# Optimization experiments

Hardware: AMD Instinct MI355X
Metric: run time of the kernel (lower is better)

## Reference

```python
import jax, jax.numpy as jnp
import numpy as np
from jax import lax

H = W = 496
K = 5            # gabor kernel size
WIN = 16         # window_size
STRIDE = 16
PATCH = 32
GAMMA = 0.5
PSI = np.pi / 2
THETAS = np.array([np.pi/8, np.pi/4, 3*np.pi/8, np.pi/2, 5*np.pi/8, 6*np.pi/8, 7*np.pi/8, np.pi], dtype=np.float32)


def setup_inputs() -> dict:
    key = jax.random.key(0)
    k1, k2, k3 = jax.random.split(key, 3)
    img = jax.random.normal(k1, (1, 1, H, W), dtype=jnp.float32)
    sigmas = jax.random.uniform(k2, (1, 3), dtype=jnp.float32) * 10.0   # nn.Parameter(rand*10)
    lambdas = jax.random.uniform(k3, (1, 3), dtype=jnp.float32) * np.pi  # nn.Parameter(rand*pi)
    return {"img": img, "sigmas": sigmas, "lambdas": lambdas}


def _gabor_bank(sigmas, lambdas):
    # axes: (sigma, lambda, theta, ky, kx)
    idx = jnp.arange(K, dtype=jnp.float32) - (K - 1) / 2.0
    sig = sigmas[0][:, None, None, None, None]          # [3,1,1,1,1]
    lam = lambdas[0][None, :, None, None, None]         # [1,3,1,1,1]
    th = jnp.asarray(THETAS)[None, None, :, None, None] # [1,1,8,1,1]
    y = idx[None, None, None, :, None]
    x = idx[None, None, None, None, :]
    sigma_x = sig
    sigma_y = sig / GAMMA
    sin_t, cos_t = jnp.sin(th), jnp.cos(th)
    y_theta = -x * sin_t + y * cos_t
    x_theta = x * cos_t + y * sin_t
    gb = jnp.exp(-0.5 * (x_theta**2 / sigma_x**2 + y_theta**2 / sigma_y**2)) \
         * jnp.cos(2.0 * np.pi * x_theta / lam + PSI)
    return gb.reshape(-1, 1, K, K)  # [72,1,5,5]


def reference(img, sigmas, lambdas):
    gb = _gabor_bank(sigmas, lambdas)
    res = lax.conv_general_dilated(
        img, gb, window_strides=(1, 1), padding=[(K // 2, K // 2)] * 2,
        dimension_numbers=("NCHW", "OIHW", "NCHW"))          # [1,72,H,W]
    res = res.reshape(1, 9, 8, H, W).max(axis=2)              # max over 8 thetas -> [1,9,H,W]
    out = res[0]                                              # [9,H,W]

    # find_maxima: per-channel threshold at 5*mean, zero below (torch.nn.Threshold)
    mean = out.mean(axis=(1, 2), keepdims=True)
    thr = jnp.where(out > mean * 5.0, out, 0.0)

    nw = H // STRIDE                                          # 31
    windows = thr.reshape(9, nw, WIN, nw, WIN).transpose(0, 1, 3, 2, 4).reshape(9, nw * nw, WIN * WIN)
    is_max = jnp.argmax(windows, axis=2) == (WIN * WIN) // 2  # [9, 961]

    w_idx = jnp.arange(nw * nw)
    rows = w_idx // nw * STRIDE + WIN // 2
    cols = w_idx % nw * STRIDE + WIN // 2

    # describe: zero-pad by 16, gather 32x32 patch at each candidate keypoint for every channel
    pad = jnp.pad(out, ((0, 0), (16, 16), (16, 16)))
    pr = rows[:, None, None] + jnp.arange(PATCH)[None, :, None]   # [961,32,1]
    pc = cols[:, None, None] + jnp.arange(PATCH)[None, None, :]   # [961,1,32]
    patches = pad[:, pr, pc]                                      # [9,961,32,32]

    # keep patches only for detected keypoints with nonzero content (original skips zero patches)
    valid_kp = jnp.any(is_max, axis=0)                            # [961]
    nonzero = jnp.any(patches != 0, axis=(2, 3))                  # [9,961]
    mask = (valid_kp[None, :] & nonzero).astype(patches.dtype)
    patches = patches * mask[:, :, None, None]
    return patches
```

## Files before the change

kernel.cpp:

```cpp
#include <hip/hip_runtime.h>
#include <math.h>

#define HH 496
#define WW 496
#define HWSZ (HH*WW)
#define NW 31
#define NWIN (NW*NW)

__constant__ float c_thetas[8] = {
    0.39269908169872414f, 0.7853981633974483f, 1.1780972450961724f,
    1.5707963267948966f,  1.9634954084936207f, 2.356194490192345f,
    2.748893571891069f,   3.141592653589793f};

__global__ void bank_kernel(const float* __restrict__ sigmas,
                            const float* __restrict__ lambdas,
                            float* __restrict__ filt,
                            float* __restrict__ meanacc) {
    int idx = threadIdx.x + blockIdx.x * blockDim.x;
    if (idx >= 1800) {
        if (idx < 1809) meanacc[(idx - 1800) * 16] = 0.0f;
        return;
    }
    int f = idx / 25, k = idx % 25;
    int dy = k / 5, dx = k % 5;
    int s = f / 24, rem = f % 24, l = rem / 8, t = rem % 8;
    float sig = sigmas[s], lam = lambdas[l], th = c_thetas[t];
    float y = (float)dy - 2.0f, x = (float)dx - 2.0f;
    float st = sinf(th), ct = cosf(th);
    float yt = -x * st + y * ct;
    float xt =  x * ct + y * st;
    float sx2 = sig * sig;
    float sy2 = 4.0f * sig * sig;
    float g = expf(-0.5f * (xt * xt / sx2 + yt * yt / sy2)) *
              cosf(6.28318530717958647692f * xt / lam + 1.5707963267948966f);
    filt[k * 72 + f] = g;
}

#define FMAS(FP, P) \
    a0  = fmaf(P, (FP)[0],  a0);  a1  = fmaf(P, (FP)[1],  a1);  \
    a2  = fmaf(P, (FP)[2],  a2);  a3  = fmaf(P, (FP)[3],  a3);  \
    a4  = fmaf(P, (FP)[4],  a4);  a5  = fmaf(P, (FP)[5],  a5);  \
    a6  = fmaf(P, (FP)[6],  a6);  a7  = fmaf(P, (FP)[7],  a7);  \
    a8  = fmaf(P, (FP)[8],  a8);  a9  = fmaf(P, (FP)[9],  a9);  \
    a10 = fmaf(P, (FP)[10], a10); a11 = fmaf(P, (FP)[11], a11); \
    a12 = fmaf(P, (FP)[12], a12); a13 = fmaf(P, (FP)[13], a13); \
    a14 = fmaf(P, (FP)[14], a14); a15 = fmaf(P, (FP)[15], a15); \
    a16 = fmaf(P, (FP)[16], a16); a17 = fmaf(P, (FP)[17], a17); \
    a18 = fmaf(P, (FP)[18], a18); a19 = fmaf(P, (FP)[19], a19); \
    a20 = fmaf(P, (FP)[20], a20); a21 = fmaf(P, (FP)[21], a21); \
    a22 = fmaf(P, (FP)[22], a22); a23 = fmaf(P, (FP)[23], a23);

#define STEP(K, DY, DX) { \
    float pix = tile[tbase + (DY)*20 + (DX)]; \
    const float* fp = fbase + (K)*72; \
    FMAS(fp, pix) }

__global__ __launch_bounds__(256) void conv_kernel(
    const float* __restrict__ img, const float* __restrict__ filt,
    float* __restrict__ out, float* __restrict__ meanacc) {
    __shared__ float tile[20 * 20];
    __shared__ float red[4][3];
    int tid = threadIdx.x;
    int tx = tid & 15, ty = tid >> 4;
    int bx = blockIdx.x, by = blockIdx.y, cg = blockIdx.z;

    for (int i = tid; i < 400; i += 256) {
        int tY = i / 20, tX = i % 20;
        int gy = by * 16 + tY - 2, gx = bx * 16 + tX - 2;
        float v = 0.0f;
        if (gy >= 0 && gy < HH && gx >= 0 && gx < WW) v = img[gy * WW + gx];
        tile[i] = v;
    }
    __syncthreads();

    float a0=0,a1=0,a2=0,a3=0,a4=0,a5=0,a6=0,a7=0,a8=0,a9=0,a10=0,a11=0,
          a12=0,a13=0,a14=0,a15=0,a16=0,a17=0,a18=0,a19=0,a20=0,a21=0,a22=0,a23=0;
    int tbase = ty * 20 + tx;
    const float* fbase = filt + cg * 24;

    STEP( 0,0,0) STEP( 1,0,1) STEP( 2,0,2) STEP( 3,0,3) STEP( 4,0,4)
    STEP( 5,1,0) STEP( 6,1,1) STEP( 7,1,2) STEP( 8,1,3) STEP( 9,1,4)
    STEP(10,2,0) STEP(11,2,1) STEP(12,2,2) STEP(13,2,3) STEP(14,2,4)
    STEP(15,3,0) STEP(16,3,1) STEP(17,3,2) STEP(18,3,3) STEP(19,3,4)
    STEP(20,4,0) STEP(21,4,1) STEP(22,4,2) STEP(23,4,3) STEP(24,4,4)

    int y = by * 16 + ty, x = bx * 16 + tx;

    float m0 = fmaxf(fmaxf(fmaxf(a0,a1),fmaxf(a2,a3)),fmaxf(fmaxf(a4,a5),fmaxf(a6,a7)));
    float m1 = fmaxf(fmaxf(fmaxf(a8,a9),fmaxf(a10,a11)),fmaxf(fmaxf(a12,a13),fmaxf(a14,a15)));
    float m2 = fmaxf(fmaxf(fmaxf(a16,a17),fmaxf(a18,a19)),fmaxf(fmaxf(a20,a21),fmaxf(a22,a23)));

    out[(cg * 3 + 0) * HWSZ + y * WW + x] = m0;
    out[(cg * 3 + 1) * HWSZ + y * WW + x] = m1;
    out[(cg * 3 + 2) * HWSZ + y * WW + x] = m2;

#define RED(CC, MV) { \
        float s = MV; \
        s += __shfl_down(s, 32, 64); s += __shfl_down(s, 16, 64); \
        s += __shfl_down(s,  8, 64); s += __shfl_down(s,  4, 64); \
        s += __shfl_down(s,  2, 64); s += __shfl_down(s,  1, 64); \
        if ((tid & 63) == 0) red[tid >> 6][CC] = s; }
    RED(0, m0) RED(1, m1) RED(2, m2)
    __syncthreads();
    if (tid < 3)
        atomicAdd(&meanacc[(cg * 3 + tid) * 16],
                  red[0][tid] + red[1][tid] + red[2][tid] + red[3][tid]);
}

__global__ __launch_bounds__(256) void patch_kernel(
    const float* __restrict__ out, const float* __restrict__ meanacc,
    float* __restrict__ dst) {
    int w = blockIdx.x;
    int r = w / NW, cl = w % NW;
    int tid = threadIdx.x;
    __shared__ int lds_and[4];
    __shared__ int lds_or[4];

    int wy = tid >> 4, wx = tid & 15;
    int rowbase = (r * 16 + wy) * WW + cl * 16 + wx;
    int cbase   = (r * 16 + 8) * WW + cl * 16;
    int okmask = 0;
#pragma unroll
    for (int c = 0; c < 9; c++) {
        float m5 = meanacc[c * 16] * (5.0f / (float)HWSZ);
        float v  = out[c * HWSZ + rowbase];
        float vc = out[c * HWSZ + cbase];
        float thr  = (v  > m5) ? v  : 0.0f;
        float thrc = (vc > m5) ? vc : 0.0f;
        bool ok = (tid < 128) ? (thr < thrc) : (thr <= thrc);
        okmask |= (ok ? 1 : 0) << c;
    }
#pragma unroll
    for (int off = 1; off < 64; off <<= 1) okmask &= __shfl_xor(okmask, off, 64);
    if ((tid & 63) == 0) lds_and[tid >> 6] = okmask;

    int i = tid >> 3;
    int jg = (tid & 7) << 2;
    int row = r * 16 + i - 8;
    int col = cl * 16 + jg - 8;
    bool inb = (row >= 0 && row < HH && col >= 0 && col + 3 < WW);
    size_t pbase = (size_t)row * WW + col;
    int nzmask = 0;
    float4 p0, p1, p2, p3, p4, p5, p6, p7, p8;
#define LOADP(C, V) { \
        V = make_float4(0.f, 0.f, 0.f, 0.f); \
        if (inb) V = *(const float4*)(out + (size_t)(C) * HWSZ + pbase); \
        if (V.x != 0.f || V.y != 0.f || V.z != 0.f || V.w != 0.f) nzmask |= 1 << (C); }
    LOADP(0,p0) LOADP(1,p1) LOADP(2,p2) LOADP(3,p3) LOADP(4,p4)
    LOADP(5,p5) LOADP(6,p6) LOADP(7,p7) LOADP(8,p8)

#pragma unroll
    for (int off = 1; off < 64; off <<= 1) nzmask |= __shfl_xor(nzmask, off, 64);
    if ((tid & 63) == 0) lds_or[tid >> 6] = nzmask;
    __syncthreads();

    int am = lds_and[0] & lds_and[1] & lds_and[2] & lds_and[3];
    int om = lds_or[0] | lds_or[1] | lds_or[2] | lds_or[3];
    bool valid = (am != 0);

    size_t dbase = (size_t)w * 1024 + i * 32 + jg;
#define STOREP(C, V) { \
        float mk = (valid && ((om >> (C)) & 1)) ? 1.0f : 0.0f; \
        V.x *= mk; V.y *= mk; V.z *= mk; V.w *= mk; \
        *(float4*)(dst + (size_t)(C) * NWIN * 1024 + dbase) = V; }
    STOREP(0,p0) STOREP(1,p1) STOREP(2,p2) STOREP(3,p3) STOREP(4,p4)
    STOREP(5,p5) STOREP(6,p6) STOREP(7,p7) STOREP(8,p8)
}

extern "C" void kernel_launch(void* const* d_in, const int* in_sizes, int n_in,
                              void* d_out, int out_size, void* d_ws, size_t ws_size,
                              hipStream_t stream) {
    const float* img     = (const float*)d_in[0];
    const float* sigmas  = (const float*)d_in[1];
    const float* lambdas = (const float*)d_in[2];
    float* ws = (float*)d_ws;
    float* filt    = ws;
    float* meanacc = ws + 2048;
    float* outb    = ws + 4096;

    bank_kernel<<<8, 256, 0, stream>>>(sigmas, lambdas, filt, meanacc);
    conv_kernel<<<dim3(NW, NW, 3), 256, 0, stream>>>(img, filt, outb, meanacc);
    patch_kernel<<<NWIN, 256, 0, stream>>>(outb, meanacc, (float*)d_out);
}
```

Baseline: 122.1 us.

## Fuse convolution and patch extraction into one cooperative kernel with grid sync

The separate conv and patch kernels are merged into one cooperative kernel launched with a fixed grid of 496 blocks of 512 threads. Each block covers two 16x16 windows and computes all 9 channel groups per thread. The per-channel mean is accumulated with atomics, and a grid-wide sync then lets the same blocks run the thresholding, argmax check and patch gather. This removes one kernel launch and the gap between kernels. In exchange, far fewer threads run the convolution, each doing three times the work, and it adds the cost of a grid barrier and of a cooperative launch.

```diff
diff --git a/kernel.cpp b/kernel.cpp
--- a/kernel.cpp
+++ b/kernel.cpp
@@ -1,5 +1,8 @@
 #include <hip/hip_runtime.h>
+#include <hip/hip_cooperative_groups.h>
 #include <math.h>
+
+namespace cg = cooperative_groups;
 
 #define HH 496
 #define WW 496
@@ -51,78 +54,93 @@
     a22 = fmaf(P, (FP)[22], a22); a23 = fmaf(P, (FP)[23], a23);
 
 #define STEP(K, DY, DX) { \
-    float pix = tile[tbase + (DY)*20 + (DX)]; \
+    float pix = mytile[tbase + (DY)*20 + (DX)]; \
     const float* fp = fbase + (K)*72; \
     FMAS(fp, pix) }
 
-__global__ __launch_bounds__(256) void conv_kernel(
+#define MAX8(B) fmaxf(fmaxf(fmaxf(a##B,a1##B... )))
+
+#define CONV_GROUP(CG, CS0, CS1, CS2) { \
+    float a0=0,a1=0,a2=0,a3=0,a4=0,a5=0,a6=0,a7=0,a8=0,a9=0,a10=0,a11=0, \
+          a12=0,a13=0,a14=0,a15=0,a16=0,a17=0,a18=0,a19=0,a20=0,a21=0,a22=0,a23=0; \
+    const float* fbase = filt + (CG)*24; \
+    STEP( 0,0,0) STEP( 1,0,1) STEP( 2,0,2) STEP( 3,0,3) STEP( 4,0,4) \
+    STEP( 5,1,0) STEP( 6,1,1) STEP( 7,1,2) STEP( 8,1,3) STEP( 9,1,4) \
+    STEP(10,2,0) STEP(11,2,1) STEP(12,2,2) STEP(13,2,3) STEP(14,2,4) \
+    STEP(15,3,0) STEP(16,3,1) STEP(17,3,2) STEP(18,3,3) STEP(19,3,4) \
+    STEP(20,4,0) STEP(21,4,1) STEP(22,4,2) STEP(23,4,3) STEP(24,4,4) \
+    CS0 = fmaxf(fmaxf(fmaxf(a0,a1),fmaxf(a2,a3)),fmaxf(fmaxf(a4,a5),fmaxf(a6,a7))); \
+    CS1 = fmaxf(fmaxf(fmaxf(a8,a9),fmaxf(a10,a11)),fmaxf(fmaxf(a12,a13),fmaxf(a14,a15))); \
+    CS2 = fmaxf(fmaxf(fmaxf(a16,a17),fmaxf(a18,a19)),fmaxf(fmaxf(a20,a21),fmaxf(a22,a23))); \
+    if (active) { \
+        out[((CG)*3+0)*HWSZ + y*WW + x] = CS0; \
+        out[((CG)*3+1)*HWSZ + y*WW + x] = CS1; \
+        out[((CG)*3+2)*HWSZ + y*WW + x] = CS2; } }
+
+#define REDC(C, V) { \
+        float s = V; \
+        s += __shfl_down(s, 32, 64); s += __shfl_down(s, 16, 64); \
+        s += __shfl_down(s,  8, 64); s += __shfl_down(s,  4, 64); \
+        s += __shfl_down(s,  2, 64); s += __shfl_down(s,  1, 64); \
+        if ((threadIdx.x & 63) == 0) red[threadIdx.x >> 6][C] = s; }
+
+__global__ __launch_bounds__(512, 4) void fused_kernel(
     const float* __restrict__ img, const float* __restrict__ filt,
-    float* __restrict__ out, float* __restrict__ meanacc) {
-    __shared__ float tile[20 * 20];
-    __shared__ float red[4][3];
-    int tid = threadIdx.x;
+    float* __restrict__ out, float* meanacc, float* __restrict__ dst) {
+    __shared__ float tile[2][400];
+    __shared__ float red[8][9];
+    __shared__ int lds_and[8];
+    __shared__ int lds_or[8];
+
+    cg::grid_group grid = cg::this_grid();
+
+    int half = threadIdx.x >> 8;
+    int tid  = threadIdx.x & 255;
+    int pair = blockIdx.x;
+    int by = pair >> 4;
+    int bx = (pair & 15) * 2 + half;
+    bool active = (bx < NW);
     int tx = tid & 15, ty = tid >> 4;
-    int bx = blockIdx.x, by = blockIdx.y, cg = blockIdx.z;
-
+
+    float* mytile = tile[half];
     for (int i = tid; i < 400; i += 256) {
         int tY = i / 20, tX = i % 20;
         int gy = by * 16 + tY - 2, gx = bx * 16 + tX - 2;
         float v = 0.0f;
         if (gy >= 0 && gy < HH && gx >= 0 && gx < WW) v = img[gy * WW + gx];
-        tile[i] = v;
+        mytile[i] = v;
     }
     __syncthreads();
 
-    float a0=0,a1=0,a2=0,a3=0,a4=0,a5=0,a6=0,a7=0,a8=0,a9=0,a10=0,a11=0,
-          a12=0,a13=0,a14=0,a15=0,a16=0,a17=0,a18=0,a19=0,a20=0,a21=0,a22=0,a23=0;
     int tbase = ty * 20 + tx;
-    const float* fbase = filt + cg * 24;
-
-    STEP( 0,0,0) STEP( 1,0,1) STEP( 2,0,2) STEP( 3,0,3) STEP( 4,0,4)
-    STEP( 5,1,0) STEP( 6,1,1) STEP( 7,1,2) STEP( 8,1,3) STEP( 9,1,4)
-    STEP(10,2,0) STEP(11,2,1) STEP(12,2,2) STEP(13,2,3) STEP(14,2,4)
-    STEP(15,3,0) STEP(16,3,1) STEP(17,3,2) STEP(18,3,3) STEP(19,3,4)
-    STEP(20,4,0) STEP(21,4,1) STEP(22,4,2) STEP(23,4,3) STEP(24,4,4)
-
     int y = by * 16 + ty, x = bx * 16 + tx;
 
-    float m0 = fmaxf(fmaxf(fmaxf(a0,a1),fmaxf(a2,a3)),fmaxf(fmaxf(a4,a5),fmaxf(a6,a7)));
-    float m1 = fmaxf(fmaxf(fmaxf(a8,a9),fmaxf(a10,a11)),fmaxf(fmaxf(a12,a13),fmaxf(a14,a15)));
-    float m2 = fmaxf(fmaxf(fmaxf(a16,a17),fmaxf(a18,a19)),fmaxf(fmaxf(a20,a21),fmaxf(a22,a23)));
-
-    out[(cg * 3 + 0) * HWSZ + y * WW + x] = m0;
-    out[(cg * 3 + 1) * HWSZ + y * WW + x] = m1;
-    out[(cg * 3 + 2) * HWSZ + y * WW + x] = m2;
-
-#define RED(CC, MV) { \
-        float s = MV; \
-        s += __shfl_down(s, 32, 64); s += __shfl_down(s, 16, 64); \
-        s += __shfl_down(s,  8, 64); s += __shfl_down(s,  4, 64); \
-        s += __shfl_down(s,  2, 64); s += __shfl_down(s,  1, 64); \
-        if ((tid & 63) == 0) red[tid >> 6][CC] = s; }
-    RED(0, m0) RED(1, m1) RED(2, m2)
+    float cs0, cs1, cs2, cs3, cs4, cs5, cs6, cs7, cs8;
+    CONV_GROUP(0, cs0, cs1, cs2)
+    CONV_GROUP(1, cs3, cs4, cs5)
+    CONV_GROUP(2, cs6, cs7, cs8)
+
+    REDC(0, cs0) REDC(1, cs1) REDC(2, cs2) REDC(3, cs3) REDC(4, cs4)
+    REDC(5, cs5) REDC(6, cs6) REDC(7, cs7) REDC(8, cs8)
     __syncthreads();
-    if (tid < 3)
-        atomicAdd(&meanacc[(cg * 3 + tid) * 16],
-                  red[0][tid] + red[1][tid] + red[2][tid] + red[3][tid]);
-}
-
-__global__ __launch_bounds__(256) void patch_kernel(
-    const float* __restrict__ out, const float* __restrict__ meanacc,
-    float* __restrict__ dst) {
-    int w = blockIdx.x;
-    int r = w / NW, cl = w % NW;
-    int tid = threadIdx.x;
-    __shared__ int lds_and[4];
-    __shared__ int lds_or[4];
-
+    if (active && tid < 9) {
+        int h4 = half * 4;
+        atomicAdd(&meanacc[tid * 16],
+                  red[h4][tid] + red[h4+1][tid] + red[h4+2][tid] + red[h4+3][tid]);
+    }
+
+    grid.sync();
+
+    int r = by, cl = bx;
     int wy = tid >> 4, wx = tid & 15;
     int rowbase = (r * 16 + wy) * WW + cl * 16 + wx;
     int cbase   = (r * 16 + 8) * WW + cl * 16;
+
+    volatile float* mv = meanacc;
     int okmask = 0;
 #pragma unroll
     for (int c = 0; c < 9; c++) {
-        float m5 = meanacc[c * 16] * (5.0f / (float)HWSZ);
+        float m5 = mv[c * 16] * (5.0f / (float)HWSZ);
         float v  = out[c * HWSZ + rowbase];
         float vc = out[c * HWSZ + cbase];
         float thr  = (v  > m5) ? v  : 0.0f;
@@ -132,13 +150,13 @@
     }
 #pragma unroll
     for (int off = 1; off < 64; off <<= 1) okmask &= __shfl_xor(okmask, off, 64);
-    if ((tid & 63) == 0) lds_and[tid >> 6] = okmask;
+    if ((threadIdx.x & 63) == 0) lds_and[threadIdx.x >> 6] = okmask;
 
     int i = tid >> 3;
     int jg = (tid & 7) << 2;
     int row = r * 16 + i - 8;
     int col = cl * 16 + jg - 8;
-    bool inb = (row >= 0 && row < HH && col >= 0 && col + 3 < WW);
+    bool inb = (row >= 0 && row < HH && col >= 0 && col + 3 < WW) && active;
     size_t pbase = (size_t)row * WW + col;
     int nzmask = 0;
     float4 p0, p1, p2, p3, p4, p5, p6, p7, p8;
@@ -151,20 +169,23 @@
 
 #pragma unroll
     for (int off = 1; off < 64; off <<= 1) nzmask |= __shfl_xor(nzmask, off, 64);
-    if ((tid & 63) == 0) lds_or[tid >> 6] = nzmask;
+    if ((threadIdx.x & 63) == 0) lds_or[threadIdx.x >> 6] = nzmask;
     __syncthreads();
 
-    int am = lds_and[0] & lds_and[1] & lds_and[2] & lds_and[3];
-    int om = lds_or[0] | lds_or[1] | lds_or[2] | lds_or[3];
-    bool valid = (am != 0);
-
-    size_t dbase = (size_t)w * 1024 + i * 32 + jg;
+    if (active) {
+        int h4 = half * 4;
+        int am = lds_and[h4] & lds_and[h4+1] & lds_and[h4+2] & lds_and[h4+3];
+        int om = lds_or[h4] | lds_or[h4+1] | lds_or[h4+2] | lds_or[h4+3];
+        bool valid = (am != 0);
+        int w = by * NW + bx;
+        size_t dbase = (size_t)w * 1024 + i * 32 + jg;
 #define STOREP(C, V) { \
         float mk = (valid && ((om >> (C)) & 1)) ? 1.0f : 0.0f; \
         V.x *= mk; V.y *= mk; V.z *= mk; V.w *= mk; \
         *(float4*)(dst + (size_t)(C) * NWIN * 1024 + dbase) = V; }
-    STOREP(0,p0) STOREP(1,p1) STOREP(2,p2) STOREP(3,p3) STOREP(4,p4)
-    STOREP(5,p5) STOREP(6,p6) STOREP(7,p7) STOREP(8,p8)
+        STOREP(0,p0) STOREP(1,p1) STOREP(2,p2) STOREP(3,p3) STOREP(4,p4)
+        STOREP(5,p5) STOREP(6,p6) STOREP(7,p7) STOREP(8,p8)
+    }
 }
 
 extern "C" void kernel_launch(void* const* d_in, const int* in_sizes, int n_in,
@@ -177,8 +198,11 @@
     float* filt    = ws;
     float* meanacc = ws + 2048;
     float* outb    = ws + 4096;
+    float* dst     = (float*)d_out;
 
     bank_kernel<<<8, 256, 0, stream>>>(sigmas, lambdas, filt, meanacc);
-    conv_kernel<<<dim3(NW, NW, 3), 256, 0, stream>>>(img, filt, outb, meanacc);
-    patch_kernel<<<NWIN, 256, 0, stream>>>(outb, meanacc, (float*)d_out);
+
+    void* args[] = {(void*)&img, (void*)&filt, (void*)&outb, (void*)&meanacc, (void*)&dst};
+    hipLaunchCooperativeKernel((const void*)fused_kernel, dim3(496), dim3(512),
+                               args, 0, stream);
 }
```

Measured after the change: 179.7 us. +47.1%, slower.
